# Kernel tuning notes

Hardware: AMD Instinct MI355X
Metric: run time of the kernel (lower is better)

## Reference

```python
import jax, jax.numpy as jnp
import numpy as np

BN_EPS = 1e-5


def conv1d_reflect(x, w, dilation, bias=None):
    # x: [N, C_in, L], w: [C_out, C_in, K]; reflect pad preserves length for K=3, pad=dilation
    k = w.shape[-1]
    p = ((k - 1) * dilation + 1) // 2
    xp = jnp.pad(x, ((0, 0), (0, 0), (p, p)), mode='reflect')
    y = jax.lax.conv_general_dilated(
        xp, w, window_strides=(1,), padding='VALID',
        rhs_dilation=(dilation,), dimension_numbers=('NCH', 'OIH', 'NCH'))
    if bias is not None:
        y = y + bias[None, :, None]
    return y


def bn_eval(x, gamma, beta, mean, var):
    inv = gamma / jnp.sqrt(var + BN_EPS)
    return x * inv[None, :, None] + (beta - mean * inv)[None, :, None]


def upsample2_linear(x):
    # F.interpolate(scale_factor=2, mode='linear', align_corners=False)
    L = x.shape[-1]
    src = (jnp.arange(2 * L, dtype=jnp.float32) + 0.5) * 0.5 - 0.5
    src = jnp.maximum(src, 0.0)
    i0 = jnp.floor(src).astype(jnp.int32)
    i1 = jnp.minimum(i0 + 1, L - 1)
    w = (src - i0.astype(jnp.float32)).astype(x.dtype)
    return x[..., i0] * (1.0 - w) + x[..., i1] * w


def setup_inputs() -> dict:
    key = jax.random.key(0)
    ks = jax.random.split(key, 6)
    bt, st, ch, nt = 16, 4, 512, 1024
    fusion = jax.random.normal(ks[0], (bt, st, ch, nt), dtype=jnp.float32)
    targets = jax.random.uniform(ks[1], (bt, 3, 4 * nt, st), dtype=jnp.float32)
    c1, c2 = 256, 32
    w1 = jax.random.normal(ks[2], (c1, ch, 3), dtype=jnp.float32) * 0.05
    w2 = jax.random.normal(ks[3], (c2, c1, 3), dtype=jnp.float32) * 0.05
    w_out = jax.random.normal(ks[4], (3, c2, 3), dtype=jnp.float32) * 0.05
    b_out = jnp.zeros((3,), dtype=jnp.float32)
    return {
        'fusion': fusion, 'targets': targets,
        'w1': w1,
        'bn1_gamma': jnp.ones((c1,), jnp.float32), 'bn1_beta': jnp.zeros((c1,), jnp.float32),
        'bn1_mean': jnp.zeros((c1,), jnp.float32), 'bn1_var': jnp.ones((c1,), jnp.float32),
        'w2': w2,
        'bn2_gamma': jnp.ones((c2,), jnp.float32), 'bn2_beta': jnp.zeros((c2,), jnp.float32),
        'bn2_mean': jnp.zeros((c2,), jnp.float32), 'bn2_var': jnp.ones((c2,), jnp.float32),
        'w_out': w_out, 'b_out': b_out,
    }


def reference(fusion, targets, w1, bn1_gamma, bn1_beta, bn1_mean, bn1_var,
              w2, bn2_gamma, bn2_beta, bn2_mean, bn2_var, w_out, b_out):
    bt, st, ch, nt = fusion.shape
    x = fusion.reshape(bt * st, ch, nt)
    x = jax.nn.relu(bn_eval(conv1d_reflect(x, w1, dilation=8), bn1_gamma, bn1_beta, bn1_mean, bn1_var))
    x = upsample2_linear(x)
    x = jax.nn.relu(bn_eval(conv1d_reflect(x, w2, dilation=16), bn2_gamma, bn2_beta, bn2_mean, bn2_var))
    x = upsample2_linear(x)
    x = conv1d_reflect(x, w_out, dilation=32, bias=b_out)
    x = x.reshape(bt, st, x.shape[1], x.shape[2])
    x = jnp.transpose(x, (0, 2, 3, 1))  # [bt, 3, 4*nt, st]

    # losses: vectorized masked CE (replaces the python double loop)
    logp = jax.nn.log_softmax(x.astype(jnp.float32), axis=1)
    valid = jnp.any(targets != 0, axis=(1, 2))  # [bt, st]
    num = jnp.sum(valid).astype(jnp.float32)
    T = targets.shape[2]
    loss = jnp.sum(-targets * logp) / (num * T)
    return x, loss
```

## Files before the change

kernel.cpp:

```cpp
#include <hip/hip_runtime.h>
#include <hip/hip_bf16.h>

#define DEV static __device__ __forceinline__

typedef short bf16x8_t __attribute__((ext_vector_type(8)));
typedef float f32x4 __attribute__((ext_vector_type(4)));

#define GLDS16(gp, lp) __builtin_amdgcn_global_load_lds( \
    (const __attribute__((address_space(1))) void*)(gp), \
    (__attribute__((address_space(3))) void*)(lp), 16, 0, 0)

DEV int reflect_idx(int q, int L) {
    q = q < 0 ? -q : q;
    q = q >= L ? 2 * L - 2 - q : q;
    return q;
}

DEV unsigned short f2bf(float f) {
    unsigned int b = __float_as_uint(f);
    unsigned int r = (b + 0x7FFFu + ((b >> 16) & 1u)) >> 16;
    return (unsigned short)r;
}
DEV float bf2f(unsigned short u) {
    return __uint_as_float(((unsigned int)u) << 16);
}

__global__ void kprep(const float* __restrict__ w1, const float* __restrict__ w2,
                      unsigned short* __restrict__ wb, unsigned short* __restrict__ w2b,
                      float* lacc) {
    int idx = blockIdx.x * 256 + threadIdx.x;
    if (idx < 393216) {
        int kk = idx >> 17;
        int rem = idx & 131071;
        int co = rem >> 9;
        int ci = rem & 511;
        wb[idx] = f2bf(w1[(co * 512 + ci) * 3 + kk]);
    } else if (idx < 417792) {
        int j = idx - 393216;
        int ci = j & 255;
        int co = (j >> 8) & 31;
        int kk = j >> 13;
        w2b[j] = f2bf(w2[(co * 256 + ci) * 3 + kk]);
    }
    if (idx < 128) lacc[idx] = 0.0f;
}

__global__ __launch_bounds__(256) void kx_t(const float* __restrict__ x,
                                            unsigned short* __restrict__ xb, int n0) {
    __shared__ float ls[64][65];
    const int tid = threadIdx.x;
    const int t0 = blockIdx.x * 64, ci0 = blockIdx.y * 64;
    const int n = n0 + blockIdx.z;
    const float* xp = x + ((size_t)n * 512 + ci0) * 1024 + t0;
    for (int idx = tid; idx < 1024; idx += 256) {
        int r = idx >> 4, c4 = (idx & 15) * 4;
        float4 v = *(const float4*)(xp + r * 1024 + c4);
        ls[r][c4] = v.x; ls[r][c4 + 1] = v.y; ls[r][c4 + 2] = v.z; ls[r][c4 + 3] = v.w;
    }
    __syncthreads();
    unsigned short* xo = xb + ((size_t)blockIdx.z * 1024 + t0) * 512 + ci0;
#pragma unroll
    for (int p = 0; p < 2; ++p) {
        int trow = (tid >> 3) + p * 32;
        int cj = (tid & 7) * 8;
        unsigned short pk[8];
#pragma unroll
        for (int j = 0; j < 8; ++j) pk[j] = f2bf(ls[cj + j][trow]);
        *(uint4*)(xo + (size_t)trow * 512 + cj) = *(const uint4*)pk;
    }
}

__global__ __launch_bounds__(256, 2) void k1_mfma(
    const unsigned short* __restrict__ xb, const unsigned short* __restrict__ wb,
    const float* __restrict__ g, const float* __restrict__ be,
    const float* __restrict__ mn, const float* __restrict__ vr,
    unsigned short* __restrict__ y1t, int n0)
{
    const int tid  = threadIdx.x;
    const int lane = tid & 63;
    const int w    = tid >> 6;
    const int tw   = w >> 1;
    const int cw   = w & 1;
    const int tq   = lane & 15;
    const int qd   = lane >> 4;
    const int t0   = blockIdx.x * 128;
    const int nr   = blockIdx.y;
    const int n    = n0 + nr;
    const int cb   = blockIdx.z;

    __shared__ unsigned short smem[32768];

    const int rl0 = tid >> 2;
    const int rl1 = 64 + (tid >> 2);
    const int q0  = (tid & 3) ^ ((rl0 >> 1) & 3);
    const int q1  = (tid & 3) ^ ((rl1 >> 1) & 3);

    const unsigned short* xn = xb + (size_t)nr * 1024 * 512;
    int aoff0[3], aoff1[3];
#pragma unroll
    for (int kk = 0; kk < 3; ++kk) {
        aoff0[kk] = reflect_idx(t0 + rl0 + 8 * kk - 8, 1024) * 512 + q0 * 8;
        aoff1[kk] = reflect_idx(t0 + rl1 + 8 * kk - 8, 1024) * 512 + q1 * 8;
    }
    const unsigned short* wp0 = wb + (size_t)(cb * 128 + rl0) * 512 + q0 * 8;
    const unsigned short* wp1 = wb + (size_t)(cb * 128 + rl1) * 512 + q1 * 8;

    const int atom = qd ^ ((tq >> 1) & 3);

    f32x4 acc[4][4];
#pragma unroll
    for (int a = 0; a < 4; ++a)
#pragma unroll
        for (int b = 0; b < 4; ++b) acc[a][b] = (f32x4){0.f, 0.f, 0.f, 0.f};

#pragma unroll
    for (int p = 0; p < 2; ++p) {
        GLDS16(xn + aoff0[0] + p * 32, &smem[p * 8192 + tid * 8]);
        GLDS16(xn + aoff1[0] + p * 32, &smem[p * 8192 + 2048 + tid * 8]);
        GLDS16(wp0 + p * 32, &smem[p * 8192 + 4096 + tid * 8]);
        GLDS16(wp1 + p * 32, &smem[p * 8192 + 6144 + tid * 8]);
    }

#pragma unroll
    for (int c = 0; c < 24; ++c) {
        const int bo = (c & 1) * 16384;
        __syncthreads();
        if (c < 23) {
            const int nc = c + 1, nk = nc >> 3, nj = nc & 7;
            const int no = ((c + 1) & 1) * 16384;
#pragma unroll
            for (int p = 0; p < 2; ++p) {
                const int col = nj * 64 + p * 32;
                GLDS16(xn + aoff0[nk] + col, &smem[no + p * 8192 + tid * 8]);
                GLDS16(xn + aoff1[nk] + col, &smem[no + p * 8192 + 2048 + tid * 8]);
                GLDS16(wp0 + (size_t)nk * 131072 + col, &smem[no + p * 8192 + 4096 + tid * 8]);
                GLDS16(wp1 + (size_t)nk * 131072 + col, &smem[no + p * 8192 + 6144 + tid * 8]);
            }
        }
#pragma unroll
        for (int p = 0; p < 2; ++p) {
            const int ab = bo + p * 8192;
            bf16x8_t Af[4], Bf[4];
#pragma unroll
            for (int ts = 0; ts < 4; ++ts)
                Af[ts] = *(const bf16x8_t*)&smem[ab + (tw * 64 + ts * 16 + tq) * 32 + atom * 8];
#pragma unroll
            for (int cs = 0; cs < 4; ++cs)
                Bf[cs] = *(const bf16x8_t*)&smem[ab + 4096 + (cw * 64 + cs * 16 + tq) * 32 + atom * 8];
#pragma unroll
            for (int ts = 0; ts < 4; ++ts)
#pragma unroll
                for (int cs = 0; cs < 4; ++cs)
                    acc[ts][cs] = __builtin_amdgcn_mfma_f32_16x16x32_bf16(
                        Af[ts], Bf[cs], acc[ts][cs], 0, 0, 0);
        }
    }

    __syncthreads();
#pragma unroll
    for (int cs = 0; cs < 4; ++cs) {
        int col = cw * 64 + cs * 16 + tq;
        int co  = cb * 128 + col;
        float iv = g[co] / sqrtf(vr[co] + 1e-5f);
        float sh = be[co] - mn[co] * iv;
#pragma unroll
        for (int ts = 0; ts < 4; ++ts)
#pragma unroll
            for (int rg = 0; rg < 4; ++rg)
                smem[(tw * 64 + ts * 16 + qd * 4 + rg) * 136 + col] =
                    f2bf(fmaxf(fmaf(acc[ts][cs][rg], iv, sh), 0.0f));
    }
    __syncthreads();
    const int srow = tid >> 4, sseg = tid & 15;
#pragma unroll
    for (int p = 0; p < 8; ++p) {
        int row = p * 16 + srow;
        unsigned short* yp = y1t + ((size_t)n * 1024 + t0 + row) * 256 + cb * 128 + sseg * 8;
        *(uint4*)yp = *(const uint4*)&smem[row * 136 + sseg * 8];
    }
}

__global__ __launch_bounds__(256, 2) void k2_mfma(
    const unsigned short* __restrict__ y1t, const unsigned short* __restrict__ w2b,
    const float* __restrict__ g, const float* __restrict__ be,
    const float* __restrict__ mn, const float* __restrict__ vr,
    float* __restrict__ y2t)
{
    const int tid  = threadIdx.x;
    const int lane = tid & 63;
    const int w    = tid >> 6;
    const int tq   = lane & 15;
    const int qd   = lane >> 4;
    const int t0   = blockIdx.x * 256;
    const int n    = blockIdx.y;

    __shared__ union SM {
        unsigned short us[2][288 * 40];
        float tr[256 * 36];
    } sm;

    f32x4 acc[4][2];
#pragma unroll
    for (int a = 0; a < 4; ++a)
#pragma unroll
        for (int b = 0; b < 2; ++b) acc[a][b] = (f32x4){0.f, 0.f, 0.f, 0.f};

    const unsigned short* yn = y1t + (size_t)n * 1024 * 256;

    auto stage = [&](int ch, int buf) {
        const int ci0 = ch * 32;
        for (int idx = tid; idx < 1152; idx += 256) {
            int r = idx >> 2, gq = idx & 3;
            int u = reflect_idx(t0 - 16 + r, 2048);
            float src = fmaxf((float)u * 0.5f - 0.25f, 0.0f);
            int i0 = (int)src;
            float wl = src - (float)i0;
            int i1 = i0 + 1 > 1023 ? 1023 : i0 + 1;
            const unsigned short* p0 = yn + (size_t)i0 * 256 + ci0 + gq * 8;
            const unsigned short* p1 = yn + (size_t)i1 * 256 + ci0 + gq * 8;
            uint4 ua = *(const uint4*)p0;
            uint4 ub = *(const uint4*)p1;
            const unsigned short* sa = (const unsigned short*)&ua;
            const unsigned short* sb = (const unsigned short*)&ub;
            unsigned short pk[8];
#pragma unroll
            for (int j = 0; j < 8; ++j) {
                float a = bf2f(sa[j]);
                float b = bf2f(sb[j]);
                pk[j] = f2bf(a + wl * (b - a));
            }
            *(uint4*)&sm.us[buf][r * 40 + gq * 8] = *(const uint4*)pk;
        }
    };

    stage(0, 0);
    for (int ch = 0; ch < 8; ++ch) {
        const int buf = ch & 1;
        __syncthreads();
        if (ch < 7) stage(ch + 1, buf ^ 1);

        const int ci0 = ch * 32;
        bf16x8_t Bf[2][3];
#pragma unroll
        for (int cs = 0; cs < 2; ++cs)
#pragma unroll
            for (int kk = 0; kk < 3; ++kk)
                Bf[cs][kk] = *(const bf16x8_t*)(w2b +
                    ((size_t)(kk * 32 + cs * 16 + tq)) * 256 + ci0 + qd * 8);

        bf16x8_t Af[6];
#pragma unroll
        for (int s = 0; s < 6; ++s)
            Af[s] = *(const bf16x8_t*)&sm.us[buf][(w * 64 + s * 16 + tq) * 40 + qd * 8];

#pragma unroll
        for (int ts = 0; ts < 4; ++ts)
#pragma unroll
            for (int cs = 0; cs < 2; ++cs)
#pragma unroll
                for (int kk = 0; kk < 3; ++kk)
                    acc[ts][cs] = __builtin_amdgcn_mfma_f32_16x16x32_bf16(
                        Af[ts + kk], Bf[cs][kk], acc[ts][cs], 0, 0, 0);
    }

    __syncthreads();
#pragma unroll
    for (int cs = 0; cs < 2; ++cs) {
        int co = cs * 16 + tq;
        float iv = g[co] / sqrtf(vr[co] + 1e-5f);
        float sh = be[co] - mn[co] * iv;
#pragma unroll
        for (int ts = 0; ts < 4; ++ts)
#pragma unroll
            for (int rg = 0; rg < 4; ++rg) {
                int tl = w * 64 + ts * 16 + qd * 4 + rg;
                sm.tr[tl * 36 + co] = fmaxf(fmaf(acc[ts][cs][rg], iv, sh), 0.0f);
            }
    }
    __syncthreads();
    float* yo = y2t + ((size_t)n * 2048 + t0 + tid) * 32;
#pragma unroll
    for (int j = 0; j < 8; ++j)
        *(float4*)(yo + j * 4) = *(const float4*)&sm.tr[tid * 36 + j * 4];
}

__global__ __launch_bounds__(256, 2) void k3_out(
    const float* __restrict__ y2t, const float* __restrict__ w3,
    const float* __restrict__ bias, float* __restrict__ out)
{
    const int tid = threadIdx.x;
    const int t0 = blockIdx.x * 256;
    const int n  = blockIdx.y;

    __shared__ float us[32 * 321];
    __shared__ float wsh[288];

    for (int idx = tid; idx < 288; idx += 256) wsh[idx] = w3[idx];

    const float* yn = y2t + (size_t)n * 2048 * 32;
    for (int idx = tid; idx < 1280; idx += 256) {
        int r = idx >> 2, gq = idx & 3;
        int u = reflect_idx(t0 - 32 + r, 4096);
        float src = fmaxf((float)u * 0.5f - 0.25f, 0.0f);
        int i0 = (int)src;
        float wl = src - (float)i0;
        int i1 = i0 + 1 > 2047 ? 2047 : i0 + 1;
        const float* p0 = yn + (size_t)i0 * 32 + gq * 8;
        const float* p1 = yn + (size_t)i1 * 32 + gq * 8;
        float4 a0 = *(const float4*)p0;
        float4 a1 = *(const float4*)(p0 + 4);
        float4 b0 = *(const float4*)p1;
        float4 b1 = *(const float4*)(p1 + 4);
        float v[8];
        v[0] = a0.x + wl * (b0.x - a0.x); v[1] = a0.y + wl * (b0.y - a0.y);
        v[2] = a0.z + wl * (b0.z - a0.z); v[3] = a0.w + wl * (b0.w - a0.w);
        v[4] = a1.x + wl * (b1.x - a1.x); v[5] = a1.y + wl * (b1.y - a1.y);
        v[6] = a1.z + wl * (b1.z - a1.z); v[7] = a1.w + wl * (b1.w - a1.w);
#pragma unroll
        for (int j = 0; j < 8; ++j)
            us[(gq * 8 + j) * 321 + r] = v[j];
    }
    __syncthreads();

    float a0 = 0.0f, a1 = 0.0f, a2 = 0.0f;
#pragma unroll 8
    for (int ci = 0; ci < 32; ++ci) {
        float x0 = us[ci * 321 + tid];
        float x1 = us[ci * 321 + tid + 32];
        float x2 = us[ci * 321 + tid + 64];
        a0 = fmaf(wsh[(0 * 32 + ci) * 3 + 0], x0, a0);
        a0 = fmaf(wsh[(0 * 32 + ci) * 3 + 1], x1, a0);
        a0 = fmaf(wsh[(0 * 32 + ci) * 3 + 2], x2, a0);
        a1 = fmaf(wsh[(1 * 32 + ci) * 3 + 0], x0, a1);
        a1 = fmaf(wsh[(1 * 32 + ci) * 3 + 1], x1, a1);
        a1 = fmaf(wsh[(1 * 32 + ci) * 3 + 2], x2, a1);
        a2 = fmaf(wsh[(2 * 32 + ci) * 3 + 0], x0, a2);
        a2 = fmaf(wsh[(2 * 32 + ci) * 3 + 1], x1, a2);
        a2 = fmaf(wsh[(2 * 32 + ci) * 3 + 2], x2, a2);
    }
    int b = n >> 2, s = n & 3;
    int t = t0 + tid;
    size_t ob = ((size_t)(b * 3) * 4096 + t) * 4 + s;
    out[ob]         = a0 + bias[0];
    out[ob + 16384] = a1 + bias[1];
    out[ob + 32768] = a2 + bias[2];
}

__global__ __launch_bounds__(256) void k4b_ce(
    const float* __restrict__ x, const float* __restrict__ tg, float* lacc)
{
    int i = blockIdx.x * 256 + threadIdx.x;
    int s = i & 3;
    int t = (i >> 2) & 4095;
    int b = i >> 14;
    size_t base = ((size_t)(b * 3) * 4096 + t) * 4 + s;
    float x0 = x[base], x1 = x[base + 16384], x2 = x[base + 32768];
    float mx = fmaxf(x0, fmaxf(x1, x2));
    float e0 = expf(x0 - mx), e1 = expf(x1 - mx), e2 = expf(x2 - mx);
    float lse = mx + logf(e0 + e1 + e2);
    float g0 = tg[base], g1 = tg[base + 16384], g2 = tg[base + 32768];
    float v = g0 * (lse - x0) + g1 * (lse - x1) + g2 * (lse - x2);
    bool nz = (g0 != 0.0f) | (g1 != 0.0f) | (g2 != 0.0f);

    __shared__ float wsum[4];
    __shared__ int sf[4];
    if (threadIdx.x < 4) sf[threadIdx.x] = 0;
    __syncthreads();
    if (nz) sf[s] = 1;

    for (int off = 32; off > 0; off >>= 1) v += __shfl_down(v, off);
    int lane = threadIdx.x & 63, wid = threadIdx.x >> 6;
    if (lane == 0) wsum[wid] = v;
    __syncthreads();
    if (threadIdx.x == 0)
        atomicAdd(lacc, wsum[0] + wsum[1] + wsum[2] + wsum[3]);
    if (threadIdx.x < 4 && sf[threadIdx.x])
        atomicOr((int*)lacc + 8 + b * 4 + threadIdx.x, 1);
}

__global__ void k4c_final(const float* lacc, float* out) {
    if (threadIdx.x == 0) {
        float sum = lacc[0];
        const int* vf = (const int*)lacc + 8;
        int num = 0;
#pragma unroll
        for (int j = 0; j < 64; ++j) num += (vf[j] != 0);
        out[786432] = sum / ((float)num * 4096.0f);
    }
}

extern "C" void kernel_launch(void* const* d_in, const int* in_sizes, int n_in,
                              void* d_out, int out_size, void* d_ws, size_t ws_size,
                              hipStream_t stream) {
    (void)in_sizes; (void)n_in; (void)out_size;
    const float* fusion  = (const float*)d_in[0];
    const float* targets = (const float*)d_in[1];
    const float* w1  = (const float*)d_in[2];
    const float* g1  = (const float*)d_in[3];
    const float* be1 = (const float*)d_in[4];
    const float* mn1 = (const float*)d_in[5];
    const float* vr1 = (const float*)d_in[6];
    const float* w2  = (const float*)d_in[7];
    const float* g2  = (const float*)d_in[8];
    const float* be2 = (const float*)d_in[9];
    const float* mn2 = (const float*)d_in[10];
    const float* vr2 = (const float*)d_in[11];
    const float* w3  = (const float*)d_in[12];
    const float* b3  = (const float*)d_in[13];
    float* out = (float*)d_out;

    char* ws = (char*)d_ws;
    unsigned short* y1t = (unsigned short*)ws;
    unsigned short* xb  = (unsigned short*)(ws + 33554432);
    float* y2t = (float*)(ws + 33554432);

    const bool single = ws_size >= 101500000ull;
    size_t woff = single ? (33554432ull + 67108864ull) : (33554432ull + 16777216ull);
    unsigned short* wb  = (unsigned short*)(ws + woff);
    unsigned short* w2b = (unsigned short*)(ws + woff + 786432);
    float* lacc = (float*)(ws + woff + 786432 + 49152);

    kprep<<<1632, 256, 0, stream>>>(w1, w2, wb, w2b, lacc);
    if (single) {
        kx_t<<<dim3(16, 8, 64), 256, 0, stream>>>(fusion, xb, 0);
        k1_mfma<<<dim3(8, 64, 2), 256, 0, stream>>>(xb, wb, g1, be1, mn1, vr1, y1t, 0);
    } else {
        for (int r = 0; r < 4; ++r) {
            kx_t<<<dim3(16, 8, 16), 256, 0, stream>>>(fusion, xb, r * 16);
            k1_mfma<<<dim3(8, 16, 2), 256, 0, stream>>>(xb, wb, g1, be1, mn1, vr1, y1t, r * 16);
        }
    }
    k2_mfma<<<dim3(8, 64), 256, 0, stream>>>(y1t, w2b, g2, be2, mn2, vr2, y2t);
    k3_out<<<dim3(16, 64), 256, 0, stream>>>(y2t, w3, b3, out);
    k4b_ce<<<1024, 256, 0, stream>>>(out, targets, lacc);
    k4c_final<<<1, 64, 0, stream>>>(lacc, out);
}
```

Baseline: 357.5 us.

## Fuse weight prep into transpose and cross-entropy plus finalize into output conv

Weight bf16 conversion and accumulator zeroing move into the input-transpose kernel, handled by the first 16 blocks with a strided loop. The softmax cross-entropy reduction is fused into the final conv kernel, so the logits are used straight from registers instead of being read back from memory. The final loss division is done by the last block to finish, detected with an atomic counter and thread fences. This removes three kernel launches and one pass over the logits, at the cost of a few straggler blocks doing extra weight-conversion work and a serialized last-block epilogue.

Result: slower. 405.9 us (+13.5%).

```diff
diff --git a/kernel.cpp b/kernel.cpp
--- a/kernel.cpp
+++ b/kernel.cpp
@@ -25,30 +25,34 @@
     return __uint_as_float(((unsigned int)u) << 16);
 }
 
-__global__ void kprep(const float* __restrict__ w1, const float* __restrict__ w2,
-                      unsigned short* __restrict__ wb, unsigned short* __restrict__ w2b,
-                      float* lacc) {
-    int idx = blockIdx.x * 256 + threadIdx.x;
-    if (idx < 393216) {
-        int kk = idx >> 17;
-        int rem = idx & 131071;
-        int co = rem >> 9;
-        int ci = rem & 511;
-        wb[idx] = f2bf(w1[(co * 512 + ci) * 3 + kk]);
-    } else if (idx < 417792) {
-        int j = idx - 393216;
-        int ci = j & 255;
-        int co = (j >> 8) & 31;
-        int kk = j >> 13;
-        w2b[j] = f2bf(w2[(co * 256 + ci) * 3 + kk]);
-    }
-    if (idx < 128) lacc[idx] = 0.0f;
-}
-
-__global__ __launch_bounds__(256) void kx_t(const float* __restrict__ x,
-                                            unsigned short* __restrict__ xb, int n0) {
+__global__ __launch_bounds__(256) void kprep_xt(
+        const float* __restrict__ x, const float* __restrict__ w1,
+        const float* __restrict__ w2, unsigned short* __restrict__ xb,
+        unsigned short* __restrict__ wb, unsigned short* __restrict__ w2b,
+        float* lacc, int n0) {
+    const int tid = threadIdx.x;
+
+    if (blockIdx.y == 0 && blockIdx.z == 0) {
+        int g = blockIdx.x * 256 + tid;
+        for (int idx = g; idx < 417792; idx += 4096) {
+            if (idx < 393216) {
+                int kk = idx >> 17;
+                int rem = idx & 131071;
+                int co = rem >> 9;
+                int ci = rem & 511;
+                wb[idx] = f2bf(w1[(co * 512 + ci) * 3 + kk]);
+            } else {
+                int j = idx - 393216;
+                int ci = j & 255;
+                int co = (j >> 8) & 31;
+                int kk = j >> 13;
+                w2b[j] = f2bf(w2[(co * 256 + ci) * 3 + kk]);
+            }
+        }
+        if (g < 128) lacc[g] = 0.0f;
+    }
+
     __shared__ float ls[64][65];
-    const int tid = threadIdx.x;
     const int t0 = blockIdx.x * 64, ci0 = blockIdx.y * 64;
     const int n = n0 + blockIdx.z;
     const float* xp = x + ((size_t)n * 512 + ci0) * 1024 + t0;
@@ -284,9 +288,10 @@
         *(float4*)(yo + j * 4) = *(const float4*)&sm.tr[tid * 36 + j * 4];
 }
 
-__global__ __launch_bounds__(256, 2) void k3_out(
+__global__ __launch_bounds__(256, 2) void k3_ce(
     const float* __restrict__ y2t, const float* __restrict__ w3,
-    const float* __restrict__ bias, float* __restrict__ out)
+    const float* __restrict__ bias, const float* __restrict__ tg,
+    float* __restrict__ out, float* lacc)
 {
     const int tid = threadIdx.x;
     const int t0 = blockIdx.x * 256;
@@ -294,6 +299,8 @@
 
     __shared__ float us[32 * 321];
     __shared__ float wsh[288];
+    __shared__ float wsum[4];
+    __shared__ int snz[4];
 
     for (int idx = tid; idx < 288; idx += 256) wsh[idx] = w3[idx];
 
@@ -341,51 +348,40 @@
     int b = n >> 2, s = n & 3;
     int t = t0 + tid;
     size_t ob = ((size_t)(b * 3) * 4096 + t) * 4 + s;
-    out[ob]         = a0 + bias[0];
-    out[ob + 16384] = a1 + bias[1];
-    out[ob + 32768] = a2 + bias[2];
-}
-
-__global__ __launch_bounds__(256) void k4b_ce(
-    const float* __restrict__ x, const float* __restrict__ tg, float* lacc)
-{
-    int i = blockIdx.x * 256 + threadIdx.x;
-    int s = i & 3;
-    int t = (i >> 2) & 4095;
-    int b = i >> 14;
-    size_t base = ((size_t)(b * 3) * 4096 + t) * 4 + s;
-    float x0 = x[base], x1 = x[base + 16384], x2 = x[base + 32768];
+    float x0 = a0 + bias[0];
+    float x1 = a1 + bias[1];
+    float x2 = a2 + bias[2];
+    out[ob]         = x0;
+    out[ob + 16384] = x1;
+    out[ob + 32768] = x2;
+
     float mx = fmaxf(x0, fmaxf(x1, x2));
     float e0 = expf(x0 - mx), e1 = expf(x1 - mx), e2 = expf(x2 - mx);
     float lse = mx + logf(e0 + e1 + e2);
-    float g0 = tg[base], g1 = tg[base + 16384], g2 = tg[base + 32768];
+    float g0 = tg[ob], g1 = tg[ob + 16384], g2 = tg[ob + 32768];
     float v = g0 * (lse - x0) + g1 * (lse - x1) + g2 * (lse - x2);
     bool nz = (g0 != 0.0f) | (g1 != 0.0f) | (g2 != 0.0f);
 
-    __shared__ float wsum[4];
-    __shared__ int sf[4];
-    if (threadIdx.x < 4) sf[threadIdx.x] = 0;
-    __syncthreads();
-    if (nz) sf[s] = 1;
-
     for (int off = 32; off > 0; off >>= 1) v += __shfl_down(v, off);
-    int lane = threadIdx.x & 63, wid = threadIdx.x >> 6;
-    if (lane == 0) wsum[wid] = v;
-    __syncthreads();
-    if (threadIdx.x == 0)
+    unsigned long long m = __ballot(nz);
+    int lane = tid & 63, wid = tid >> 6;
+    if (lane == 0) { wsum[wid] = v; snz[wid] = (m != 0ull); }
+    __syncthreads();
+    if (tid == 0) {
         atomicAdd(lacc, wsum[0] + wsum[1] + wsum[2] + wsum[3]);
-    if (threadIdx.x < 4 && sf[threadIdx.x])
-        atomicOr((int*)lacc + 8 + b * 4 + threadIdx.x, 1);
-}
-
-__global__ void k4c_final(const float* lacc, float* out) {
-    if (threadIdx.x == 0) {
-        float sum = lacc[0];
-        const int* vf = (const int*)lacc + 8;
-        int num = 0;
-#pragma unroll
-        for (int j = 0; j < 64; ++j) num += (vf[j] != 0);
-        out[786432] = sum / ((float)num * 4096.0f);
+        if (snz[0] | snz[1] | snz[2] | snz[3])
+            atomicOr((int*)lacc + 8 + n, 1);
+        __threadfence();
+        int done = atomicAdd((int*)lacc + 120, 1);
+        if (done == (int)(gridDim.x * gridDim.y) - 1) {
+            __threadfence();
+            float sum = atomicAdd(lacc, 0.0f);
+            int num = 0;
+#pragma unroll
+            for (int j = 0; j < 64; ++j)
+                num += (atomicOr((int*)lacc + 8 + j, 0) != 0);
+            out[786432] = sum / ((float)num * 4096.0f);
+        }
     }
 }
 
@@ -420,18 +416,15 @@
     unsigned short* w2b = (unsigned short*)(ws + woff + 786432);
     float* lacc = (float*)(ws + woff + 786432 + 49152);
 
-    kprep<<<1632, 256, 0, stream>>>(w1, w2, wb, w2b, lacc);
     if (single) {
-        kx_t<<<dim3(16, 8, 64), 256, 0, stream>>>(fusion, xb, 0);
+        kprep_xt<<<dim3(16, 8, 64), 256, 0, stream>>>(fusion, w1, w2, xb, wb, w2b, lacc, 0);
         k1_mfma<<<dim3(8, 64, 2), 256, 0, stream>>>(xb, wb, g1, be1, mn1, vr1, y1t, 0);
     } else {
         for (int r = 0; r < 4; ++r) {
-            kx_t<<<dim3(16, 8, 16), 256, 0, stream>>>(fusion, xb, r * 16);
+            kprep_xt<<<dim3(16, 8, 16), 256, 0, stream>>>(fusion, w1, w2, xb, wb, w2b, lacc, r * 16);
             k1_mfma<<<dim3(8, 16, 2), 256, 0, stream>>>(xb, wb, g1, be1, mn1, vr1, y1t, r * 16);
         }
     }
     k2_mfma<<<dim3(8, 64), 256, 0, stream>>>(y1t, w2b, g2, be2, mn2, vr2, y2t);
-    k3_out<<<dim3(16, 64), 256, 0, stream>>>(y2t, w3, b3, out);
-    k4b_ce<<<1024, 256, 0, stream>>>(out, targets, lacc);
-    k4c_final<<<1, 64, 0, stream>>>(lacc, out);
-}
+    k3_ce<<<dim3(16, 64), 256, 0, stream>>>(y2t, w3, b3, targets, out, lacc);
+}
```
